# Performance work log

Hardware: AMD Instinct MI355X
Metric: run time of the kernel (lower is better)

The kernel has to match this reference:

```python
import jax, jax.numpy as jnp
import numpy as np

B, S, H = 32, 1024, 768          # batch, seq_len, bert hidden
E, W, P = 128, 8, 512            # entities/sample, span width, rel pairs/sample
NT, NR = 5, 9                    # entity types, relation types
D1, HEADS1, D2, RD = 128, 2, 64, 32
REL_IN = 2 * D2 + RD + H         # 928


def _layernorm(x, g, b):
    m = x.mean(-1, keepdims=True)
    v = x.var(-1, keepdims=True)
    return (x - m) * jax.lax.rsqrt(v + 1e-5) * g + b


def _gat_dense(x, Wm, a_src, a_dst, bias, concat):
    # Fully-connected entity graph (incl. self-loops, PyG GATConv default).
    Bn, En, _ = x.shape
    Hh, D = a_src.shape
    h = (x @ Wm).reshape(Bn, En, Hh, D)                      # [B,E,h,D]
    s = jnp.einsum('behd,hd->beh', h, a_src)                 # source score
    d = jnp.einsum('behd,hd->beh', h, a_dst)                 # target score
    # edge j->i : e_ij = leaky_relu(s_j + d_i)
    e = jax.nn.leaky_relu(d[:, :, None, :] + s[:, None, :, :], 0.2)  # [B,i,j,h]
    alpha = jax.nn.softmax(e, axis=2)
    o = jnp.einsum('bijh,bjhd->bihd', alpha, h)
    o = o.reshape(Bn, En, Hh * D) if concat else o.mean(axis=2)
    return o + bias


def setup_inputs() -> dict:
    key = jax.random.key(0)
    ks = jax.random.split(key, 20)
    f = lambda k, shape: jax.random.normal(k, shape, jnp.float32) * 0.02
    return dict(
        sequence_output=jax.random.normal(ks[0], (B, S, H), jnp.float32),
        entity_starts=jax.random.randint(ks[1], (B, E), 0, S - W),
        entity_type_ids=jax.random.randint(ks[2], (B, E), 0, NT),
        pair_idx=jax.random.randint(ks[3], (B, P, 2), 0, E),
        rel_type_ids=jax.random.randint(ks[4], (B, P), 0, NR),
        entity_type_emb=f(ks[5], (NT, H)),
        rel_type_emb=f(ks[6], (NR, RD)),
        W1=f(ks[7], (H, HEADS1 * D1)), a_src1=f(ks[8], (HEADS1, D1)),
        a_dst1=f(ks[9], (HEADS1, D1)), b1=jnp.zeros((HEADS1 * D1,), jnp.float32),
        ln1_g=jnp.ones((HEADS1 * D1,), jnp.float32), ln1_b=jnp.zeros((HEADS1 * D1,), jnp.float32),
        W2=f(ks[10], (HEADS1 * D1, D2)), a_src2=f(ks[11], (1, D2)),
        a_dst2=f(ks[12], (1, D2)), b2=jnp.zeros((D2,), jnp.float32),
        ln2_g=jnp.ones((D2,), jnp.float32), ln2_b=jnp.zeros((D2,), jnp.float32),
        Wr1=f(ks[13], (REL_IN, 256)), br1=jnp.zeros((256,), jnp.float32),
        Wr2=f(ks[14], (256, 1)), br2=jnp.zeros((1,), jnp.float32),
    )


def reference(sequence_output, entity_starts, entity_type_ids, pair_idx, rel_type_ids,
              entity_type_emb, rel_type_emb,
              W1, a_src1, a_dst1, b1, ln1_g, ln1_b,
              W2, a_src2, a_dst2, b2, ln2_g, ln2_b,
              Wr1, br1, Wr2, br2):
    bidx = jnp.arange(B)[:, None]
    # --- per-entity attention pooling over span tokens ---
    tok_idx = entity_starts[:, :, None] + jnp.arange(W)            # [B,E,W]
    toks = sequence_output[jnp.arange(B)[:, None, None], tok_idx]  # [B,E,W,H]
    mean = toks.mean(axis=2)                                       # [B,E,H]
    attn = jax.nn.softmax(jnp.einsum('bewh,beh->bew', toks, mean), axis=-1)
    pooled = jnp.einsum('bew,bewh->beh', attn, toks)
    x = pooled + entity_type_emb[entity_type_ids]                  # [B,E,H]
    # --- 2-layer GAT over fully-connected entity graph ---
    x = jax.nn.elu(_layernorm(_gat_dense(x, W1, a_src1, a_dst1, b1, True), ln1_g, ln1_b))
    x = jax.nn.elu(_layernorm(_gat_dense(x, W2, a_src2, a_dst2, b2, False), ln2_g, ln2_b))
    # --- gather-concat relation MLP scoring ---
    cls = sequence_output[:, 0, :]                                 # [B,H]
    x1 = x[bidx, pair_idx[:, :, 0]]                                # [B,P,64]
    x2 = x[bidx, pair_idx[:, :, 1]]
    rel = rel_type_emb[rel_type_ids]                               # [B,P,32]
    pv = jnp.concatenate([x1, x2, rel, jnp.broadcast_to(cls[:, None, :], (B, P, H))], axis=-1)
    scores = (jax.nn.relu(pv @ Wr1 + br1) @ Wr2 + br2)[..., 0]     # [B,P]
    return scores
```

## Files before the change

### kernel.cpp

```cpp
#include <hip/hip_runtime.h>
#include <hip/hip_bf16.h>

#define BB 32
#define SS 1024
#define HHH 768
#define EE 128
#define WW 8
#define PP 512
#define RDD 32

typedef __attribute__((ext_vector_type(8))) short bf16x8;
typedef __attribute__((ext_vector_type(8))) unsigned short us8;
typedef __attribute__((ext_vector_type(4))) unsigned short us4;
typedef __attribute__((ext_vector_type(4))) float f32x4;

__device__ __forceinline__ unsigned short f2bf(float v) {
    __hip_bfloat16 h = __float2bfloat16(v);
    return *(unsigned short*)&h;
}

__global__ __launch_bounds__(256) void pool_prep_kernel(
    const float* __restrict__ seq, const int* __restrict__ starts,
    const int* __restrict__ types, const float* __restrict__ temb,
    unsigned short* __restrict__ xout,
    const float* __restrict__ W1, unsigned short* __restrict__ Wt,
    const float* __restrict__ Wr1, unsigned short* __restrict__ Wtr,
    const float* __restrict__ W2, unsigned short* __restrict__ W2t,
    const float* __restrict__ remb, unsigned short* __restrict__ rembb,
    float* __restrict__ basep) {
    int tid = threadIdx.x;
    __shared__ float sbuf[WW * HHH];
    __shared__ float scred[WW];
    __shared__ float attn_s[WW];

    if (blockIdx.x < BB * EE) {
        int be = blockIdx.x;
        int b = be >> 7;
        int start = starts[be];
        const float4* bp4 = (const float4*)(seq + ((size_t)b * SS + start) * HHH);
        for (int idx = tid; idx < WW * (HHH / 4); idx += 256) {
            int w = idx / (HHH / 4), h4 = idx % (HHH / 4);
            float4 v = bp4[(size_t)w * (HHH / 4) + h4];
            sbuf[w * HHH + h4 * 4 + 0] = v.x; sbuf[w * HHH + h4 * 4 + 1] = v.y;
            sbuf[w * HHH + h4 * 4 + 2] = v.z; sbuf[w * HHH + h4 * 4 + 3] = v.w;
        }
        __syncthreads();

        float sc[WW];
#pragma unroll
        for (int w = 0; w < WW; w++) sc[w] = 0.f;
#pragma unroll
        for (int c = 0; c < 3; c++) {
            int h = tid + 256 * c;
            float s = 0.f;
#pragma unroll
            for (int w = 0; w < WW; w++) s += sbuf[w * HHH + h];
            float m = s * (1.0f / WW);
#pragma unroll
            for (int w = 0; w < WW; w++) sc[w] += sbuf[w * HHH + h] * m;
        }
        if (tid < WW) scred[tid] = 0.f;
        __syncthreads();
        int lane = tid & 63;
#pragma unroll
        for (int w = 0; w < WW; w++) {
            float v = sc[w];
            for (int o = 32; o > 0; o >>= 1) v += __shfl_down(v, o, 64);
            if (lane == 0) atomicAdd(&scred[w], v);
        }
        __syncthreads();
        if (tid == 0) {
            float mx = scred[0];
            for (int w = 1; w < WW; w++) mx = fmaxf(mx, scred[w]);
            float ssum = 0.f;
            float a[WW];
            for (int w = 0; w < WW; w++) { a[w] = __expf(scred[w] - mx); ssum += a[w]; }
            float inv = 1.f / ssum;
            for (int w = 0; w < WW; w++) attn_s[w] = a[w] * inv;
        }
        __syncthreads();

        int t = types[be];
        const float* emb = temb + (size_t)t * HHH;
#pragma unroll
        for (int c = 0; c < 3; c++) {
            int h = tid + 256 * c;
            float p = 0.f;
#pragma unroll
            for (int w = 0; w < WW; w++) p += attn_s[w] * sbuf[w * HHH + h];
            xout[(size_t)be * HHH + h] = f2bf(p + emb[h]);
        }
        return;
    }

    int blk = blockIdx.x - BB * EE;
    if (blk < 48) {
        int k0 = blk * 16;
        for (int i = tid; i < 16 * 256; i += 256)
            sbuf[i] = W1[(size_t)(k0 + (i >> 8)) * 256 + (i & 255)];
        __syncthreads();
        int n = tid;
        us8 v0, v1;
#pragma unroll
        for (int kk = 0; kk < 8; kk++) v0[kk] = f2bf(sbuf[kk * 256 + n]);
#pragma unroll
        for (int kk = 0; kk < 8; kk++) v1[kk] = f2bf(sbuf[(8 + kk) * 256 + n]);
        *(us8*)(Wt + (size_t)n * HHH + k0) = v0;
        *(us8*)(Wt + (size_t)n * HHH + k0 + 8) = v1;
    } else if (blk < 58) {
        int k0 = (blk - 48) * 16;
        for (int i = tid; i < 16 * 256; i += 256)
            sbuf[i] = Wr1[(size_t)(k0 + (i >> 8)) * 256 + (i & 255)];
        __syncthreads();
        int n = tid;
        us8 v0, v1;
#pragma unroll
        for (int kk = 0; kk < 8; kk++) v0[kk] = f2bf(sbuf[kk * 256 + n]);
#pragma unroll
        for (int kk = 0; kk < 8; kk++) v1[kk] = f2bf(sbuf[(8 + kk) * 256 + n]);
        *(us8*)(Wtr + (size_t)n * 160 + k0) = v0;
        *(us8*)(Wtr + (size_t)n * 160 + k0 + 8) = v1;
    } else if (blk < 74) {
        int k0 = (blk - 58) * 16;
        for (int i = tid; i < 16 * 64; i += 256)
            sbuf[(i >> 6) * 64 + (i & 63)] = W2[(size_t)(k0 + (i >> 6)) * 64 + (i & 63)];
        __syncthreads();
        if (tid < 64) {
            int n = tid;
            us8 v0, v1;
#pragma unroll
            for (int kk = 0; kk < 8; kk++) v0[kk] = f2bf(sbuf[kk * 64 + n]);
#pragma unroll
            for (int kk = 0; kk < 8; kk++) v1[kk] = f2bf(sbuf[(8 + kk) * 64 + n]);
            *(us8*)(W2t + (size_t)n * 256 + k0) = v0;
            *(us8*)(W2t + (size_t)n * 256 + k0 + 8) = v1;
        }
    } else if (blk == 74) {
        for (int i = tid; i < 9 * RDD; i += 256) rembb[i] = f2bf(remb[i]);
    } else {
        int pc = blk - 75;
        int kc = pc % 12;
        int b = pc / 12;
        int n = tid;
        if (n < 64) sbuf[4096 + n] = seq[(size_t)b * SS * HHH + kc * 64 + n];
        __syncthreads();
        float acc = 0.f;
        const float* w = Wr1 + (size_t)(160 + kc * 64) * 256 + n;
#pragma unroll 16
        for (int k = 0; k < 64; k++) acc += sbuf[4096 + k] * w[(size_t)k * 256];
        basep[((size_t)kc * 32 + b) * 256 + n] = acc;
    }
}

__global__ __launch_bounds__(256) void gemm1_mfma_kernel(
    const unsigned short* __restrict__ Xb, const unsigned short* __restrict__ Wt,
    const float* __restrict__ asrc1, const float* __restrict__ adst1,
    unsigned short* __restrict__ h1Tg,
    float* __restrict__ ps_s, float* __restrict__ ps_d) {
    const int K = HHH;
    int n0 = blockIdx.x * 64;
    int m0 = blockIdx.y * 64;
    int tid = threadIdx.x;
    int wave = tid >> 6, lane = tid & 63;
    int wm = (wave >> 1) * 32, wn = (wave & 1) * 32;

    __shared__ __align__(16) unsigned short As[64][40];
    __shared__ __align__(16) unsigned short Bs[64][40];
    __shared__ __align__(16) unsigned short T[64][72];
    __shared__ float sdred[64][2][2];

    f32x4 acc[2][2] = {};
    int ar = tid >> 2;
    int ac = (tid & 3) * 8;
    int fr = lane & 15;
    int fk = (lane >> 4) * 8;

    for (int k0 = 0; k0 < K; k0 += 32) {
        us8 av = *(const us8*)(Xb + (size_t)(m0 + ar) * K + k0 + ac);
        us8 bv = *(const us8*)(Wt + (size_t)(n0 + ar) * K + k0 + ac);
        *(us8*)(&As[ar][ac]) = av;
        *(us8*)(&Bs[ar][ac]) = bv;
        __syncthreads();

        bf16x8 a0 = *(const bf16x8*)(&As[wm + fr][fk]);
        bf16x8 a1 = *(const bf16x8*)(&As[wm + 16 + fr][fk]);
        bf16x8 b0 = *(const bf16x8*)(&Bs[wn + fr][fk]);
        bf16x8 b1 = *(const bf16x8*)(&Bs[wn + 16 + fr][fk]);

        acc[0][0] = __builtin_amdgcn_mfma_f32_16x16x32_bf16(a0, b0, acc[0][0], 0, 0, 0);
        acc[0][1] = __builtin_amdgcn_mfma_f32_16x16x32_bf16(a0, b1, acc[0][1], 0, 0, 0);
        acc[1][0] = __builtin_amdgcn_mfma_f32_16x16x32_bf16(a1, b0, acc[1][0], 0, 0, 0);
        acc[1][1] = __builtin_amdgcn_mfma_f32_16x16x32_bf16(a1, b1, acc[1][1], 0, 0, 0);
        __syncthreads();
    }

    int crow = (lane >> 4) * 4;
    int ccol = lane & 15;
    int h = n0 >> 7;
    int nb = (n0 >> 6) & 1;
    int dbase = (n0 & 127) + wn;

    float asv[2], adv[2];
#pragma unroll
    for (int ni = 0; ni < 2; ni++) {
        int d = dbase + ni * 16 + ccol;
        asv[ni] = asrc1[h * 128 + d];
        adv[ni] = adst1[h * 128 + d];
    }

#pragma unroll
    for (int mi = 0; mi < 2; mi++) {
#pragma unroll
        for (int r = 0; r < 4; r++) {
            float sp = 0.f, dp = 0.f;
#pragma unroll
            for (int ni = 0; ni < 2; ni++) {
                float v = acc[mi][ni][r];
                T[wn + ni * 16 + ccol][wm + mi * 16 + crow + r] = f2bf(v);
                sp += v * asv[ni];
                dp += v * adv[ni];
            }
            for (int msk = 1; msk < 16; msk <<= 1) {
                sp += __shfl_xor(sp, msk, 64);
                dp += __shfl_xor(dp, msk, 64);
            }
            if ((lane & 15) == 0) {
                int row = wm + mi * 16 + crow + r;
                sdred[row][wn >> 5][0] = sp;
                sdred[row][wn >> 5][1] = dp;
            }
        }
    }
    __syncthreads();

    int b = m0 >> 7;
    int j0 = m0 & 127;
    if (tid < 64) {
        float spt = sdred[tid][0][0] + sdred[tid][1][0];
        float dpt = sdred[tid][0][1] + sdred[tid][1][1];
        size_t o = (size_t)nb * 8192 + ((size_t)(m0 + tid)) * 2 + h;
        ps_s[o] = spt;
        ps_d[o] = dpt;
    }
    {
        int d_l = tid >> 2, q = tid & 3;
        us8 v0 = *(const us8*)(&T[d_l][q * 16]);
        us8 v1 = *(const us8*)(&T[d_l][q * 16 + 8]);
        size_t go = ((size_t)(b * 2 + h) * 128 + (n0 & 127) + d_l) * 128 + j0 + q * 16;
        *(us8*)(h1Tg + go) = v0;
        *(us8*)(h1Tg + go + 8) = v1;
    }
}

__global__ __launch_bounds__(256) void gat1_gemm2_kernel(
    const unsigned short* __restrict__ h1Tg,
    const float* __restrict__ ps_s, const float* __restrict__ ps_d,
    const float* __restrict__ b1, const float* __restrict__ gamma,
    const float* __restrict__ beta,
    const unsigned short* __restrict__ W2t,
    const float* __restrict__ asrc2, const float* __restrict__ adst2,
    unsigned short* __restrict__ h2Tg, float* __restrict__ s2,
    float* __restrict__ d2) {
    int b = blockIdx.x >> 2;
    int c = blockIdx.x & 3;
    int tid = threadIdx.x;
    int wave = tid >> 6, lane = tid & 63;
    int h = wave >> 1, m = wave & 1;
    int fr = lane & 15;
    int fk = (lane >> 4) * 8;

    __shared__ __align__(16) unsigned short h1T[2][128][136];
    __shared__ float ssh[2][128];
    __shared__ float dsh[2][128];
    __shared__ float lnred[32][2][2];
    __shared__ __align__(16) unsigned short g1s[32][264];
    __shared__ float sdr2[32][2][2];
    __shared__ __align__(16) unsigned short t2[64][40];

    {
        const us8* src = (const us8*)(h1Tg + (size_t)b * 32768);
#pragma unroll
        for (int it = 0; it < 16; it++) {
            int i8 = tid + it * 256;
            int row = i8 >> 4;
            int j8 = i8 & 15;
            *(us8*)(&h1T[row >> 7][row & 127][j8 * 8]) = src[i8];
        }
        int hh = tid >> 7, j = tid & 127;
        size_t o = ((size_t)b * 128 + j) * 2 + hh;
        ssh[hh][j] = ps_s[o] + ps_s[o + 8192];
        dsh[hh][j] = ps_d[o] + ps_d[o + 8192];
    }
    __syncthreads();

    bf16x8 afrag[4];
    {
        float dd = dsh[h][c * 32 + m * 16 + fr];
        float ev[4][8];
        float mx = -1e30f;
#pragma unroll
        for (int ks = 0; ks < 4; ks++)
#pragma unroll
            for (int jj = 0; jj < 8; jj++) {
                float e = dd + ssh[h][ks * 32 + fk + jj];
                e = e >= 0.f ? e : 0.2f * e;
                ev[ks][jj] = e;
                mx = fmaxf(mx, e);
            }
        mx = fmaxf(mx, __shfl_xor(mx, 16, 64));
        mx = fmaxf(mx, __shfl_xor(mx, 32, 64));
        float sm = 0.f;
#pragma unroll
        for (int ks = 0; ks < 4; ks++)
#pragma unroll
            for (int jj = 0; jj < 8; jj++) {
                float e = __expf(ev[ks][jj] - mx);
                ev[ks][jj] = e;
                sm += e;
            }
        sm += __shfl_xor(sm, 16, 64);
        sm += __shfl_xor(sm, 32, 64);
        float inv = 1.f / sm;
#pragma unroll
        for (int ks = 0; ks < 4; ks++) {
            bf16x8 a;
#pragma unroll
            for (int jj = 0; jj < 8; jj++)
                a[jj] = (short)f2bf(ev[ks][jj] * inv);
            afrag[ks] = a;
        }
    }

    f32x4 acc[8] = {};
#pragma unroll
    for (int ks = 0; ks < 4; ks++)
#pragma unroll
        for (int ni = 0; ni < 8; ni++) {
            bf16x8 bv = *(const bf16x8*)(&h1T[h][ni * 16 + fr][ks * 32 + fk]);
            acc[ni] = __builtin_amdgcn_mfma_f32_16x16x32_bf16(
                afrag[ks], bv, acc[ni], 0, 0, 0);
        }

    int crow = (lane >> 4) * 4;
    int ccol = lane & 15;
    float bv_[8], gv[8], bev[8];
#pragma unroll
    for (int ni = 0; ni < 8; ni++) {
        int d = h * 128 + ni * 16 + ccol;
        bv_[ni] = b1[d]; gv[ni] = gamma[d]; bev[ni] = beta[d];
    }
    float vv[4][8];
#pragma unroll
    for (int r = 0; r < 4; r++) {
        float s = 0.f, q = 0.f;
#pragma unroll
        for (int ni = 0; ni < 8; ni++) {
            float v = acc[ni][r] + bv_[ni];
            vv[r][ni] = v;
            s += v;
            q += v * v;
        }
        s += __shfl_xor(s, 1, 64); s += __shfl_xor(s, 2, 64);
        s += __shfl_xor(s, 4, 64); s += __shfl_xor(s, 8, 64);
        q += __shfl_xor(q, 1, 64); q += __shfl_xor(q, 2, 64);
        q += __shfl_xor(q, 4, 64); q += __shfl_xor(q, 8, 64);
        if ((lane & 15) == 0) {
            lnred[m * 16 + crow + r][h][0] = s;
            lnred[m * 16 + crow + r][h][1] = q;
        }
    }
    __syncthreads();
#pragma unroll
    for (int r = 0; r < 4; r++) {
        int row = m * 16 + crow + r;
        float s = lnred[row][0][0] + lnred[row][1][0];
        float q = lnred[row][0][1] + lnred[row][1][1];
        float mean = s * (1.f / 256.f);
        float var = q * (1.f / 256.f) - mean * mean;
        float rs = rsqrtf(var + 1e-5f);
#pragma unroll
        for (int ni = 0; ni < 8; ni++) {
            float y = (vv[r][ni] - mean) * rs * gv[ni] + bev[ni];
            y = y > 0.f ? y : (__expf(y) - 1.f);
            g1s[row][h * 128 + ni * 16 + ccol] = f2bf(y);
        }
    }
    __syncthreads();

    int m2 = wave & 1;
    int nb = wave >> 1;
    f32x4 acc2[2] = {};
#pragma unroll
    for (int kc = 0; kc < 8; kc++) {
        bf16x8 a = *(const bf16x8*)(&g1s[m2 * 16 + fr][kc * 32 + fk]);
#pragma unroll
        for (int ni = 0; ni < 2; ni++) {
            bf16x8 wv = *(const bf16x8*)(W2t + (size_t)(nb * 32 + ni * 16 + fr) * 256 +
                                         kc * 32 + fk);
            acc2[ni] = __builtin_amdgcn_mfma_f32_16x16x32_bf16(a, wv, acc2[ni], 0, 0, 0);
        }
    }
    float as2[2], ad2[2];
#pragma unroll
    for (int ni = 0; ni < 2; ni++) {
        int n = nb * 32 + ni * 16 + ccol;
        as2[ni] = asrc2[n];
        ad2[ni] = adst2[n];
    }
#pragma unroll
    for (int r = 0; r < 4; r++) {
        int rl = m2 * 16 + crow + r;
        float sp = 0.f, dp = 0.f;
#pragma unroll
        for (int ni = 0; ni < 2; ni++) {
            float v = acc2[ni][r];
            t2[nb * 32 + ni * 16 + ccol][rl] = f2bf(v);
            sp += v * as2[ni];
            dp += v * ad2[ni];
        }
        for (int msk = 1; msk < 16; msk <<= 1) {
            sp += __shfl_xor(sp, msk, 64);
            dp += __shfl_xor(dp, msk, 64);
        }
        if ((lane & 15) == 0) {
            sdr2[rl][nb][0] = sp;
            sdr2[rl][nb][1] = dp;
        }
    }
    __syncthreads();
    if (tid < 32) {
        s2[(size_t)b * 128 + c * 32 + tid] = sdr2[tid][0][0] + sdr2[tid][1][0];
        d2[(size_t)b * 128 + c * 32 + tid] = sdr2[tid][0][1] + sdr2[tid][1][1];
    }
    {
        int d = tid >> 2, q = tid & 3;
        us8 v = *(const us8*)(&t2[d][q * 8]);
        *(us8*)(h2Tg + ((size_t)b * 64 + d) * 128 + c * 32 + q * 8) = v;
    }
}

__global__ __launch_bounds__(256) void gat2_fused_kernel(
    const unsigned short* __restrict__ h2Tg, const float* __restrict__ s2,
    const float* __restrict__ d2, const float* __restrict__ b2v,
    const float* __restrict__ gamma, const float* __restrict__ beta,
    unsigned short* __restrict__ x2b) {
    int b = blockIdx.x >> 1;
    int c = blockIdx.x & 1;
    int tid = threadIdx.x;
    int wave = tid >> 6, lane = tid & 63;
    int fr = lane & 15;
    int fk = (lane >> 4) * 8;

    __shared__ __align__(16) unsigned short h2T[64][136];
    __shared__ float ssh[128];
    __shared__ float dsh[128];

    {
        const us8* src = (const us8*)(h2Tg + (size_t)b * 64 * 128);
#pragma unroll
        for (int it = 0; it < 4; it++) {
            int i8 = tid + it * 256;
            int row = i8 >> 4;
            int j8 = i8 & 15;
            *(us8*)(&h2T[row][j8 * 8]) = src[i8];
        }
        if (tid < 128) ssh[tid] = s2[(size_t)b * 128 + tid];
        else dsh[tid - 128] = d2[(size_t)b * 128 + (tid - 128)];
    }
    __syncthreads();

    bf16x8 afrag[4];
    {
        float dd = dsh[c * 64 + wave * 16 + fr];
        float ev[4][8];
        float mx = -1e30f;
#pragma unroll
        for (int ks = 0; ks < 4; ks++)
#pragma unroll
            for (int jj = 0; jj < 8; jj++) {
                float e = dd + ssh[ks * 32 + fk + jj];
                e = e >= 0.f ? e : 0.2f * e;
                ev[ks][jj] = e;
                mx = fmaxf(mx, e);
            }
        mx = fmaxf(mx, __shfl_xor(mx, 16, 64));
        mx = fmaxf(mx, __shfl_xor(mx, 32, 64));
        float sm = 0.f;
#pragma unroll
        for (int ks = 0; ks < 4; ks++)
#pragma unroll
            for (int jj = 0; jj < 8; jj++) {
                float e = __expf(ev[ks][jj] - mx);
                ev[ks][jj] = e;
                sm += e;
            }
        sm += __shfl_xor(sm, 16, 64);
        sm += __shfl_xor(sm, 32, 64);
        float inv = 1.f / sm;
#pragma unroll
        for (int ks = 0; ks < 4; ks++) {
            bf16x8 a;
#pragma unroll
            for (int jj = 0; jj < 8; jj++)
                a[jj] = (short)f2bf(ev[ks][jj] * inv);
            afrag[ks] = a;
        }
    }

    f32x4 acc[4] = {};
#pragma unroll
    for (int ks = 0; ks < 4; ks++)
#pragma unroll
        for (int ni = 0; ni < 4; ni++) {
            bf16x8 bv = *(const bf16x8*)(&h2T[ni * 16 + fr][ks * 32 + fk]);
            acc[ni] = __builtin_amdgcn_mfma_f32_16x16x32_bf16(
                afrag[ks], bv, acc[ni], 0, 0, 0);
        }

    int crow = (lane >> 4) * 4;
    int ccol = lane & 15;
    float bv_[4], gv[4], bev[4];
#pragma unroll
    for (int ni = 0; ni < 4; ni++) {
        int d = ni * 16 + ccol;
        bv_[ni] = b2v[d]; gv[ni] = gamma[d]; bev[ni] = beta[d];
    }
#pragma unroll
    for (int r = 0; r < 4; r++) {
        float v[4];
        float s = 0.f;
#pragma unroll
        for (int ni = 0; ni < 4; ni++) {
            v[ni] = acc[ni][r] + bv_[ni];
            s += v[ni];
        }
        s += __shfl_xor(s, 1, 64); s += __shfl_xor(s, 2, 64);
        s += __shfl_xor(s, 4, 64); s += __shfl_xor(s, 8, 64);
        float mean = s * (1.f / 64.f);
        float sq = 0.f;
#pragma unroll
        for (int ni = 0; ni < 4; ni++) {
            float dv = v[ni] - mean;
            sq += dv * dv;
        }
        sq += __shfl_xor(sq, 1, 64); sq += __shfl_xor(sq, 2, 64);
        sq += __shfl_xor(sq, 4, 64); sq += __shfl_xor(sq, 8, 64);
        float rs = rsqrtf(sq * (1.f / 64.f) + 1e-5f);
        int i = c * 64 + wave * 16 + crow + r;
        unsigned short* dst = x2b + (size_t)(b * 128 + i) * 64;
#pragma unroll
        for (int ni = 0; ni < 4; ni++) {
            float y = (v[ni] - mean) * rs * gv[ni] + bev[ni];
            y = y > 0.f ? y : (__expf(y) - 1.f);
            dst[ni * 16 + ccol] = f2bf(y);
        }
    }
}

__global__ __launch_bounds__(256) void score_mfma_kernel(
    const unsigned short* __restrict__ x2b, const float* __restrict__ basep,
    const float* __restrict__ br1,
    const int* __restrict__ pair_idx, const int* __restrict__ rel_ids,
    const unsigned short* __restrict__ rembb, const unsigned short* __restrict__ Wtr,
    const float* __restrict__ Wr2, const float* __restrict__ br2,
    float* __restrict__ out) {
    int blk = blockIdx.x;
    int b = blk >> 3;
    int p0 = (blk & 7) * 64;
    int tid = threadIdx.x;
    int wave = tid >> 6, lane = tid & 63;
    int wn = wave * 64;

    __shared__ __align__(16) unsigned short As[64][168];
    __shared__ __align__(16) unsigned short Bs[256][40];
    __shared__ float sred[64][4];
    __shared__ int prs[64][3];

    if (tid < 64) {
        int p = p0 + tid;
        prs[tid][0] = pair_idx[((size_t)b * PP + p) * 2 + 0];
        prs[tid][1] = pair_idx[((size_t)b * PP + p) * 2 + 1];
        prs[tid][2] = rel_ids[(size_t)b * PP + p];
    }
    __syncthreads();
    for (int it = 0; it < 10; it++) {
        int idx = tid + it * 256;
        int m = idx / 40, c = idx % 40;
        int k0 = c * 4;
        us4 v;
        if (k0 < 64)
            v = *(const us4*)(x2b + ((size_t)b * EE + prs[m][0]) * 64 + k0);
        else if (k0 < 128)
            v = *(const us4*)(x2b + ((size_t)b * EE + prs[m][1]) * 64 + (k0 - 64));
        else
            v = *(const us4*)(rembb + prs[m][2] * RDD + (k0 - 128));
        *(us4*)(&As[m][k0]) = v;
    }

    f32x4 acc[4][4] = {};
    int fr = lane & 15;
    int fk = (lane >> 4) * 8;

    for (int kc = 0; kc < 5; kc++) {
        for (int it = 0; it < 4; it++) {
            int i = tid + it * 256;
            int n = i >> 2, c = i & 3;
            *(us8*)(&Bs[n][c * 8]) =
                *(const us8*)(Wtr + (size_t)n * 160 + kc * 32 + c * 8);
        }
        __syncthreads();
        bf16x8 a[4], bv[4];
#pragma unroll
        for (int mi = 0; mi < 4; mi++)
            a[mi] = *(const bf16x8*)(&As[mi * 16 + fr][kc * 32 + fk]);
#pragma unroll
        for (int ni = 0; ni < 4; ni++)
            bv[ni] = *(const bf16x8*)(&Bs[wn + ni * 16 + fr][fk]);
#pragma unroll
        for (int mi = 0; mi < 4; mi++)
#pragma unroll
            for (int ni = 0; ni < 4; ni++)
                acc[mi][ni] = __builtin_amdgcn_mfma_f32_16x16x32_bf16(
                    a[mi], bv[ni], acc[mi][ni], 0, 0, 0);
        __syncthreads();
    }

    int crow = (lane >> 4) * 4;
    int ccol = lane & 15;
    float basev[4], w2v[4];
#pragma unroll
    for (int ni = 0; ni < 4; ni++) {
        int n = wn + ni * 16 + ccol;
        float bb = br1[n];
#pragma unroll
        for (int kc = 0; kc < 12; kc++)
            bb += basep[((size_t)kc * 32 + b) * 256 + n];
        basev[ni] = bb;
        w2v[ni] = Wr2[n];
    }
#pragma unroll
    for (int mi = 0; mi < 4; mi++) {
#pragma unroll
        for (int r = 0; r < 4; r++) {
            float p = 0.f;
#pragma unroll
            for (int ni = 0; ni < 4; ni++)
                p += fmaxf(acc[mi][ni][r] + basev[ni], 0.f) * w2v[ni];
            for (int msk = 1; msk < 16; msk <<= 1)
                p += __shfl_xor(p, msk, 64);
            if ((lane & 15) == 0)
                sred[mi * 16 + crow + r][wave] = p;
        }
    }
    __syncthreads();
    if (tid < 64) {
        float s = sred[tid][0] + sred[tid][1] + sred[tid][2] + sred[tid][3] + br2[0];
        out[(size_t)b * PP + p0 + tid] = s;
    }
}

extern "C" void kernel_launch(void* const* d_in, const int* in_sizes, int n_in,
                              void* d_out, int out_size, void* d_ws, size_t ws_size,
                              hipStream_t stream) {
    (void)in_sizes; (void)n_in; (void)out_size; (void)ws_size;
    const float* seq      = (const float*)d_in[0];
    const int*   starts   = (const int*)d_in[1];
    const int*   types    = (const int*)d_in[2];
    const int*   pair_idx = (const int*)d_in[3];
    const int*   rel_ids  = (const int*)d_in[4];
    const float* temb     = (const float*)d_in[5];
    const float* remb     = (const float*)d_in[6];
    const float* W1       = (const float*)d_in[7];
    const float* a_src1   = (const float*)d_in[8];
    const float* a_dst1   = (const float*)d_in[9];
    const float* b1       = (const float*)d_in[10];
    const float* ln1_g    = (const float*)d_in[11];
    const float* ln1_b    = (const float*)d_in[12];
    const float* W2       = (const float*)d_in[13];
    const float* a_src2   = (const float*)d_in[14];
    const float* a_dst2   = (const float*)d_in[15];
    const float* b2       = (const float*)d_in[16];
    const float* ln2_g    = (const float*)d_in[17];
    const float* ln2_b    = (const float*)d_in[18];
    const float* Wr1      = (const float*)d_in[19];
    const float* br1      = (const float*)d_in[20];
    const float* Wr2      = (const float*)d_in[21];
    const float* br2      = (const float*)d_in[22];
    float* out = (float*)d_out;

    unsigned short* xb    = (unsigned short*)d_ws;
    unsigned short* Wt    = xb + (size_t)4096 * 768;
    unsigned short* Wtr   = Wt + (size_t)256 * 768;
    unsigned short* W2t   = Wtr + (size_t)256 * 160;
    unsigned short* rembb = W2t + (size_t)64 * 256;
    unsigned short* h1Tg  = rembb + 512;
    unsigned short* h2Tg  = h1Tg + (size_t)4096 * 256;
    unsigned short* x2b   = h2Tg + (size_t)32 * 64 * 128;
    float* fbase = (float*)(x2b + (size_t)4096 * 64);
    float* ps_s  = fbase;
    float* ps_d  = ps_s + 2 * 8192;
    float* s2    = ps_d + 2 * 8192;
    float* d2    = s2 + 4096;
    float* basep = d2 + 4096;

    pool_prep_kernel<<<BB * EE + 75 + 12 * 32, 256, 0, stream>>>(
        seq, starts, types, temb, xb, W1, Wt, Wr1, Wtr, W2, W2t, remb, rembb, basep);
    gemm1_mfma_kernel<<<dim3(4, 64), 256, 0, stream>>>(xb, Wt, a_src1, a_dst1,
                                                       h1Tg, ps_s, ps_d);
    gat1_gemm2_kernel<<<BB * 4, 256, 0, stream>>>(h1Tg, ps_s, ps_d, b1, ln1_g, ln1_b,
                                                  W2t, a_src2, a_dst2, h2Tg, s2, d2);
    gat2_fused_kernel<<<BB * 2, 256, 0, stream>>>(h2Tg, s2, d2, b2, ln2_g, ln2_b, x2b);
    score_mfma_kernel<<<BB * PP / 64, 256, 0, stream>>>(x2b, basep, br1, pair_idx,
                                                        rel_ids, rembb, Wtr, Wr2,
                                                        br2, out);
}
```

Before: 228.9 us.

## Fuse four post-pooling kernels into one cooperative kernel with grid syncs

Merges the gemm1, GAT layer 1 + gemm2, GAT layer 2 and relation-scoring kernels into a single cooperative launch of 256 blocks. Each stage reuses a shared-memory union and is separated by grid-wide syncs instead of kernel boundaries. The aim is to remove the launch overhead and tail gaps of four small kernels. In exchange, the later stages must run on a fixed 256-block grid, and every grid sync carries a cost.

```diff
diff --git a/kernel.cpp b/kernel.cpp
--- a/kernel.cpp
+++ b/kernel.cpp
@@ -1,5 +1,8 @@
 #include <hip/hip_runtime.h>
 #include <hip/hip_bf16.h>
+#include <hip/hip_cooperative_groups.h>
+
+namespace cg = cooperative_groups;
 
 #define BB 32
 #define SS 1024
@@ -152,510 +155,509 @@
     }
 }
 
-__global__ __launch_bounds__(256) void gemm1_mfma_kernel(
-    const unsigned short* __restrict__ Xb, const unsigned short* __restrict__ Wt,
-    const float* __restrict__ asrc1, const float* __restrict__ adst1,
-    unsigned short* __restrict__ h1Tg,
-    float* __restrict__ ps_s, float* __restrict__ ps_d) {
-    const int K = HHH;
-    int n0 = blockIdx.x * 64;
-    int m0 = blockIdx.y * 64;
-    int tid = threadIdx.x;
-    int wave = tid >> 6, lane = tid & 63;
-    int wm = (wave >> 1) * 32, wn = (wave & 1) * 32;
-
-    __shared__ __align__(16) unsigned short As[64][40];
-    __shared__ __align__(16) unsigned short Bs[64][40];
-    __shared__ __align__(16) unsigned short T[64][72];
-    __shared__ float sdred[64][2][2];
-
-    f32x4 acc[2][2] = {};
-    int ar = tid >> 2;
-    int ac = (tid & 3) * 8;
-    int fr = lane & 15;
-    int fk = (lane >> 4) * 8;
-
-    for (int k0 = 0; k0 < K; k0 += 32) {
-        us8 av = *(const us8*)(Xb + (size_t)(m0 + ar) * K + k0 + ac);
-        us8 bv = *(const us8*)(Wt + (size_t)(n0 + ar) * K + k0 + ac);
-        *(us8*)(&As[ar][ac]) = av;
-        *(us8*)(&Bs[ar][ac]) = bv;
-        __syncthreads();
-
-        bf16x8 a0 = *(const bf16x8*)(&As[wm + fr][fk]);
-        bf16x8 a1 = *(const bf16x8*)(&As[wm + 16 + fr][fk]);
-        bf16x8 b0 = *(const bf16x8*)(&Bs[wn + fr][fk]);
-        bf16x8 b1 = *(const bf16x8*)(&Bs[wn + 16 + fr][fk]);
-
-        acc[0][0] = __builtin_amdgcn_mfma_f32_16x16x32_bf16(a0, b0, acc[0][0], 0, 0, 0);
-        acc[0][1] = __builtin_amdgcn_mfma_f32_16x16x32_bf16(a0, b1, acc[0][1], 0, 0, 0);
-        acc[1][0] = __builtin_amdgcn_mfma_f32_16x16x32_bf16(a1, b0, acc[1][0], 0, 0, 0);
-        acc[1][1] = __builtin_amdgcn_mfma_f32_16x16x32_bf16(a1, b1, acc[1][1], 0, 0, 0);
-        __syncthreads();
-    }
-
-    int crow = (lane >> 4) * 4;
-    int ccol = lane & 15;
-    int h = n0 >> 7;
-    int nb = (n0 >> 6) & 1;
-    int dbase = (n0 & 127) + wn;
-
-    float asv[2], adv[2];
-#pragma unroll
-    for (int ni = 0; ni < 2; ni++) {
-        int d = dbase + ni * 16 + ccol;
-        asv[ni] = asrc1[h * 128 + d];
-        adv[ni] = adst1[h * 128 + d];
-    }
-
-#pragma unroll
-    for (int mi = 0; mi < 2; mi++) {
-#pragma unroll
-        for (int r = 0; r < 4; r++) {
-            float sp = 0.f, dp = 0.f;
-#pragma unroll
-            for (int ni = 0; ni < 2; ni++) {
-                float v = acc[mi][ni][r];
-                T[wn + ni * 16 + ccol][wm + mi * 16 + crow + r] = f2bf(v);
-                sp += v * asv[ni];
-                dp += v * adv[ni];
-            }
-            for (int msk = 1; msk < 16; msk <<= 1) {
-                sp += __shfl_xor(sp, msk, 64);
-                dp += __shfl_xor(dp, msk, 64);
-            }
-            if ((lane & 15) == 0) {
-                int row = wm + mi * 16 + crow + r;
-                sdred[row][wn >> 5][0] = sp;
-                sdred[row][wn >> 5][1] = dp;
-            }
-        }
-    }
-    __syncthreads();
-
-    int b = m0 >> 7;
-    int j0 = m0 & 127;
-    if (tid < 64) {
-        float spt = sdred[tid][0][0] + sdred[tid][1][0];
-        float dpt = sdred[tid][0][1] + sdred[tid][1][1];
-        size_t o = (size_t)nb * 8192 + ((size_t)(m0 + tid)) * 2 + h;
-        ps_s[o] = spt;
-        ps_d[o] = dpt;
-    }
-    {
-        int d_l = tid >> 2, q = tid & 3;
-        us8 v0 = *(const us8*)(&T[d_l][q * 16]);
-        us8 v1 = *(const us8*)(&T[d_l][q * 16 + 8]);
-        size_t go = ((size_t)(b * 2 + h) * 128 + (n0 & 127) + d_l) * 128 + j0 + q * 16;
-        *(us8*)(h1Tg + go) = v0;
-        *(us8*)(h1Tg + go + 8) = v1;
-    }
-}
-
-__global__ __launch_bounds__(256) void gat1_gemm2_kernel(
-    const unsigned short* __restrict__ h1Tg,
-    const float* __restrict__ ps_s, const float* __restrict__ ps_d,
-    const float* __restrict__ b1, const float* __restrict__ gamma,
-    const float* __restrict__ beta,
-    const unsigned short* __restrict__ W2t,
-    const float* __restrict__ asrc2, const float* __restrict__ adst2,
-    unsigned short* __restrict__ h2Tg, float* __restrict__ s2,
-    float* __restrict__ d2) {
-    int b = blockIdx.x >> 2;
-    int c = blockIdx.x & 3;
-    int tid = threadIdx.x;
-    int wave = tid >> 6, lane = tid & 63;
-    int h = wave >> 1, m = wave & 1;
-    int fr = lane & 15;
-    int fk = (lane >> 4) * 8;
-
-    __shared__ __align__(16) unsigned short h1T[2][128][136];
-    __shared__ float ssh[2][128];
-    __shared__ float dsh[2][128];
-    __shared__ float lnred[32][2][2];
-    __shared__ __align__(16) unsigned short g1s[32][264];
-    __shared__ float sdr2[32][2][2];
-    __shared__ __align__(16) unsigned short t2[64][40];
-
-    {
-        const us8* src = (const us8*)(h1Tg + (size_t)b * 32768);
-#pragma unroll
-        for (int it = 0; it < 16; it++) {
-            int i8 = tid + it * 256;
-            int row = i8 >> 4;
-            int j8 = i8 & 15;
-            *(us8*)(&h1T[row >> 7][row & 127][j8 * 8]) = src[i8];
-        }
-        int hh = tid >> 7, j = tid & 127;
-        size_t o = ((size_t)b * 128 + j) * 2 + hh;
-        ssh[hh][j] = ps_s[o] + ps_s[o + 8192];
-        dsh[hh][j] = ps_d[o] + ps_d[o + 8192];
-    }
-    __syncthreads();
-
-    bf16x8 afrag[4];
-    {
-        float dd = dsh[h][c * 32 + m * 16 + fr];
-        float ev[4][8];
-        float mx = -1e30f;
-#pragma unroll
-        for (int ks = 0; ks < 4; ks++)
-#pragma unroll
-            for (int jj = 0; jj < 8; jj++) {
-                float e = dd + ssh[h][ks * 32 + fk + jj];
-                e = e >= 0.f ? e : 0.2f * e;
-                ev[ks][jj] = e;
-                mx = fmaxf(mx, e);
-            }
-        mx = fmaxf(mx, __shfl_xor(mx, 16, 64));
-        mx = fmaxf(mx, __shfl_xor(mx, 32, 64));
-        float sm = 0.f;
-#pragma unroll
-        for (int ks = 0; ks < 4; ks++)
-#pragma unroll
-            for (int jj = 0; jj < 8; jj++) {
-                float e = __expf(ev[ks][jj] - mx);
-                ev[ks][jj] = e;
-                sm += e;
-            }
-        sm += __shfl_xor(sm, 16, 64);
-        sm += __shfl_xor(sm, 32, 64);
-        float inv = 1.f / sm;
-#pragma unroll
-        for (int ks = 0; ks < 4; ks++) {
-            bf16x8 a;
-#pragma unroll
-            for (int jj = 0; jj < 8; jj++)
-                a[jj] = (short)f2bf(ev[ks][jj] * inv);
-            afrag[ks] = a;
-        }
-    }
-
-    f32x4 acc[8] = {};
-#pragma unroll
-    for (int ks = 0; ks < 4; ks++)
-#pragma unroll
-        for (int ni = 0; ni < 8; ni++) {
-            bf16x8 bv = *(const bf16x8*)(&h1T[h][ni * 16 + fr][ks * 32 + fk]);
-            acc[ni] = __builtin_amdgcn_mfma_f32_16x16x32_bf16(
-                afrag[ks], bv, acc[ni], 0, 0, 0);
-        }
-
-    int crow = (lane >> 4) * 4;
-    int ccol = lane & 15;
-    float bv_[8], gv[8], bev[8];
-#pragma unroll
-    for (int ni = 0; ni < 8; ni++) {
-        int d = h * 128 + ni * 16 + ccol;
-        bv_[ni] = b1[d]; gv[ni] = gamma[d]; bev[ni] = beta[d];
-    }
-    float vv[4][8];
-#pragma unroll
-    for (int r = 0; r < 4; r++) {
-        float s = 0.f, q = 0.f;
-#pragma unroll
-        for (int ni = 0; ni < 8; ni++) {
-            float v = acc[ni][r] + bv_[ni];
-            vv[r][ni] = v;
-            s += v;
-            q += v * v;
-        }
-        s += __shfl_xor(s, 1, 64); s += __shfl_xor(s, 2, 64);
-        s += __shfl_xor(s, 4, 64); s += __shfl_xor(s, 8, 64);
-        q += __shfl_xor(q, 1, 64); q += __shfl_xor(q, 2, 64);
-        q += __shfl_xor(q, 4, 64); q += __shfl_xor(q, 8, 64);
-        if ((lane & 15) == 0) {
-            lnred[m * 16 + crow + r][h][0] = s;
-            lnred[m * 16 + crow + r][h][1] = q;
-        }
-    }
-    __syncthreads();
-#pragma unroll
-    for (int r = 0; r < 4; r++) {
-        int row = m * 16 + crow + r;
-        float s = lnred[row][0][0] + lnred[row][1][0];
-        float q = lnred[row][0][1] + lnred[row][1][1];
-        float mean = s * (1.f / 256.f);
-        float var = q * (1.f / 256.f) - mean * mean;
-        float rs = rsqrtf(var + 1e-5f);
-#pragma unroll
-        for (int ni = 0; ni < 8; ni++) {
-            float y = (vv[r][ni] - mean) * rs * gv[ni] + bev[ni];
-            y = y > 0.f ? y : (__expf(y) - 1.f);
-            g1s[row][h * 128 + ni * 16 + ccol] = f2bf(y);
-        }
-    }
-    __syncthreads();
-
-    int m2 = wave & 1;
-    int nb = wave >> 1;
-    f32x4 acc2[2] = {};
-#pragma unroll
-    for (int kc = 0; kc < 8; kc++) {
-        bf16x8 a = *(const bf16x8*)(&g1s[m2 * 16 + fr][kc * 32 + fk]);
-#pragma unroll
-        for (int ni = 0; ni < 2; ni++) {
-            bf16x8 wv = *(const bf16x8*)(W2t + (size_t)(nb * 32 + ni * 16 + fr) * 256 +
-                                         kc * 32 + fk);
-            acc2[ni] = __builtin_amdgcn_mfma_f32_16x16x32_bf16(a, wv, acc2[ni], 0, 0, 0);
-        }
-    }
-    float as2[2], ad2[2];
-#pragma unroll
-    for (int ni = 0; ni < 2; ni++) {
-        int n = nb * 32 + ni * 16 + ccol;
-        as2[ni] = asrc2[n];
-        ad2[ni] = adst2[n];
-    }
-#pragma unroll
-    for (int r = 0; r < 4; r++) {
-        int rl = m2 * 16 + crow + r;
-        float sp = 0.f, dp = 0.f;
-#pragma unroll
-        for (int ni = 0; ni < 2; ni++) {
-            float v = acc2[ni][r];
-            t2[nb * 32 + ni * 16 + ccol][rl] = f2bf(v);
-            sp += v * as2[ni];
-            dp += v * ad2[ni];
-        }
-        for (int msk = 1; msk < 16; msk <<= 1) {
-            sp += __shfl_xor(sp, msk, 64);
-            dp += __shfl_xor(dp, msk, 64);
-        }
-        if ((lane & 15) == 0) {
-            sdr2[rl][nb][0] = sp;
-            sdr2[rl][nb][1] = dp;
-        }
-    }
-    __syncthreads();
-    if (tid < 32) {
-        s2[(size_t)b * 128 + c * 32 + tid] = sdr2[tid][0][0] + sdr2[tid][1][0];
-        d2[(size_t)b * 128 + c * 32 + tid] = sdr2[tid][0][1] + sdr2[tid][1][1];
-    }
-    {
-        int d = tid >> 2, q = tid & 3;
-        us8 v = *(const us8*)(&t2[d][q * 8]);
-        *(us8*)(h2Tg + ((size_t)b * 64 + d) * 128 + c * 32 + q * 8) = v;
-    }
-}
-
-__global__ __launch_bounds__(256) void gat2_fused_kernel(
-    const unsigned short* __restrict__ h2Tg, const float* __restrict__ s2,
-    const float* __restrict__ d2, const float* __restrict__ b2v,
-    const float* __restrict__ gamma, const float* __restrict__ beta,
-    unsigned short* __restrict__ x2b) {
-    int b = blockIdx.x >> 1;
-    int c = blockIdx.x & 1;
+struct SmP1 {
+    unsigned short As[64][40];
+    unsigned short Bs[64][40];
+    unsigned short T[64][72];
+    float sdred[64][2][2];
+};
+struct SmP2 {
+    float ssh[2][128];
+    float dsh[2][128];
+    float lnred[32][2][2];
+    unsigned short g1s[32][264];
+    float sdr2[32][2][2];
+    unsigned short t2[64][40];
+};
+struct SmP3 {
+    float ssh[128];
+    float dsh[128];
+};
+struct SmP4 {
+    unsigned short As[64][168];
+    unsigned short Bs[256][40];
+    float sred[64][4];
+    int prs[64][3];
+};
+union SmU {
+    SmP1 p1;
+    SmP2 p2;
+    SmP3 p3;
+    SmP4 p4;
+};
+
+struct FusedParams {
+    const unsigned short* Xb;
+    const unsigned short* Wt;
+    const float* asrc1;
+    const float* adst1;
+    unsigned short* h1Tg;
+    float* ps_s;
+    float* ps_d;
+    const float* b1;
+    const float* ln1g;
+    const float* ln1b;
+    const unsigned short* W2t;
+    const float* asrc2;
+    const float* adst2;
+    unsigned short* h2Tg;
+    float* s2;
+    float* d2;
+    const float* b2v;
+    const float* ln2g;
+    const float* ln2b;
+    unsigned short* x2b;
+    const float* basep;
+    const float* br1;
+    const int* pair_idx;
+    const int* rel_ids;
+    const unsigned short* rembb;
+    const unsigned short* Wtr;
+    const float* Wr2;
+    const float* br2;
+    float* out;
+};
+
+__global__ __launch_bounds__(256) void fused_mid_kernel(FusedParams p) {
+    __shared__ __align__(16) SmU sm;
+    cg::grid_group grid = cg::this_grid();
+    int bid = blockIdx.x;
     int tid = threadIdx.x;
     int wave = tid >> 6, lane = tid & 63;
     int fr = lane & 15;
     int fk = (lane >> 4) * 8;
-
-    __shared__ __align__(16) unsigned short h2T[64][136];
-    __shared__ float ssh[128];
-    __shared__ float dsh[128];
-
-    {
-        const us8* src = (const us8*)(h2Tg + (size_t)b * 64 * 128);
-#pragma unroll
-        for (int it = 0; it < 4; it++) {
-            int i8 = tid + it * 256;
-            int row = i8 >> 4;
-            int j8 = i8 & 15;
-            *(us8*)(&h2T[row][j8 * 8]) = src[i8];
-        }
-        if (tid < 128) ssh[tid] = s2[(size_t)b * 128 + tid];
-        else dsh[tid - 128] = d2[(size_t)b * 128 + (tid - 128)];
-    }
-    __syncthreads();
-
-    bf16x8 afrag[4];
-    {
-        float dd = dsh[c * 64 + wave * 16 + fr];
-        float ev[4][8];
-        float mx = -1e30f;
-#pragma unroll
-        for (int ks = 0; ks < 4; ks++)
-#pragma unroll
-            for (int jj = 0; jj < 8; jj++) {
-                float e = dd + ssh[ks * 32 + fk + jj];
-                e = e >= 0.f ? e : 0.2f * e;
-                ev[ks][jj] = e;
-                mx = fmaxf(mx, e);
-            }
-        mx = fmaxf(mx, __shfl_xor(mx, 16, 64));
-        mx = fmaxf(mx, __shfl_xor(mx, 32, 64));
-        float sm = 0.f;
-#pragma unroll
-        for (int ks = 0; ks < 4; ks++)
-#pragma unroll
-            for (int jj = 0; jj < 8; jj++) {
-                float e = __expf(ev[ks][jj] - mx);
-                ev[ks][jj] = e;
-                sm += e;
-            }
-        sm += __shfl_xor(sm, 16, 64);
-        sm += __shfl_xor(sm, 32, 64);
-        float inv = 1.f / sm;
-#pragma unroll
-        for (int ks = 0; ks < 4; ks++) {
-            bf16x8 a;
-#pragma unroll
-            for (int jj = 0; jj < 8; jj++)
-                a[jj] = (short)f2bf(ev[ks][jj] * inv);
-            afrag[ks] = a;
-        }
-    }
-
-    f32x4 acc[4] = {};
-#pragma unroll
-    for (int ks = 0; ks < 4; ks++)
-#pragma unroll
-        for (int ni = 0; ni < 4; ni++) {
-            bf16x8 bv = *(const bf16x8*)(&h2T[ni * 16 + fr][ks * 32 + fk]);
-            acc[ni] = __builtin_amdgcn_mfma_f32_16x16x32_bf16(
-                afrag[ks], bv, acc[ni], 0, 0, 0);
-        }
-
     int crow = (lane >> 4) * 4;
     int ccol = lane & 15;
-    float bv_[4], gv[4], bev[4];
-#pragma unroll
-    for (int ni = 0; ni < 4; ni++) {
-        int d = ni * 16 + ccol;
-        bv_[ni] = b2v[d]; gv[ni] = gamma[d]; bev[ni] = beta[d];
+
+    {
+        const int K = HHH;
+        int n0 = (bid & 3) * 64;
+        int m0 = (bid >> 2) * 64;
+        int wm = (wave >> 1) * 32, wn = (wave & 1) * 32;
+
+        f32x4 acc[2][2] = {};
+        int ar = tid >> 2;
+        int ac = (tid & 3) * 8;
+
+        for (int k0 = 0; k0 < K; k0 += 32) {
+            us8 av = *(const us8*)(p.Xb + (size_t)(m0 + ar) * K + k0 + ac);
+            us8 bv = *(const us8*)(p.Wt + (size_t)(n0 + ar) * K + k0 + ac);
+            *(us8*)(&sm.p1.As[ar][ac]) = av;
+            *(us8*)(&sm.p1.Bs[ar][ac]) = bv;
+            __syncthreads();
+
+            bf16x8 a0 = *(const bf16x8*)(&sm.p1.As[wm + fr][fk]);
+            bf16x8 a1 = *(const bf16x8*)(&sm.p1.As[wm + 16 + fr][fk]);
+            bf16x8 b0 = *(const bf16x8*)(&sm.p1.Bs[wn + fr][fk]);
+            bf16x8 b1 = *(const bf16x8*)(&sm.p1.Bs[wn + 16 + fr][fk]);
+
+            acc[0][0] = __builtin_amdgcn_mfma_f32_16x16x32_bf16(a0, b0, acc[0][0], 0, 0, 0);
+            acc[0][1] = __builtin_amdgcn_mfma_f32_16x16x32_bf16(a0, b1, acc[0][1], 0, 0, 0);
+            acc[1][0] = __builtin_amdgcn_mfma_f32_16x16x32_bf16(a1, b0, acc[1][0], 0, 0, 0);
+            acc[1][1] = __builtin_amdgcn_mfma_f32_16x16x32_bf16(a1, b1, acc[1][1], 0, 0, 0);
+            __syncthreads();
+        }
+
+        int h = n0 >> 7;
+        int nb = (n0 >> 6) & 1;
+        int dbase = (n0 & 127) + wn;
+
+        float asv[2], adv[2];
+#pragma unroll
+        for (int ni = 0; ni < 2; ni++) {
+            int d = dbase + ni * 16 + ccol;
+            asv[ni] = p.asrc1[h * 128 + d];
+            adv[ni] = p.adst1[h * 128 + d];
+        }
+
+#pragma unroll
+        for (int mi = 0; mi < 2; mi++) {
+#pragma unroll
+            for (int r = 0; r < 4; r++) {
+                float sp = 0.f, dp = 0.f;
+#pragma unroll
+                for (int ni = 0; ni < 2; ni++) {
+                    float v = acc[mi][ni][r];
+                    sm.p1.T[wn + ni * 16 + ccol][wm + mi * 16 + crow + r] = f2bf(v);
+                    sp += v * asv[ni];
+                    dp += v * adv[ni];
+                }
+                for (int msk = 1; msk < 16; msk <<= 1) {
+                    sp += __shfl_xor(sp, msk, 64);
+                    dp += __shfl_xor(dp, msk, 64);
+                }
+                if ((lane & 15) == 0) {
+                    int row = wm + mi * 16 + crow + r;
+                    sm.p1.sdred[row][wn >> 5][0] = sp;
+                    sm.p1.sdred[row][wn >> 5][1] = dp;
+                }
+            }
+        }
+        __syncthreads();
+
+        int b = m0 >> 7;
+        int j0 = m0 & 127;
+        if (tid < 64) {
+            float spt = sm.p1.sdred[tid][0][0] + sm.p1.sdred[tid][1][0];
+            float dpt = sm.p1.sdred[tid][0][1] + sm.p1.sdred[tid][1][1];
+            size_t o = (size_t)nb * 8192 + ((size_t)(m0 + tid)) * 2 + h;
+            p.ps_s[o] = spt;
+            p.ps_d[o] = dpt;
+        }
+        {
+            int d_l = tid >> 2, q = tid & 3;
+            us8 v0 = *(const us8*)(&sm.p1.T[d_l][q * 16]);
+            us8 v1 = *(const us8*)(&sm.p1.T[d_l][q * 16 + 8]);
+            size_t go = ((size_t)(b * 2 + h) * 128 + (n0 & 127) + d_l) * 128 + j0 + q * 16;
+            *(us8*)(p.h1Tg + go) = v0;
+            *(us8*)(p.h1Tg + go + 8) = v1;
+        }
     }
-#pragma unroll
-    for (int r = 0; r < 4; r++) {
-        float v[4];
-        float s = 0.f;
+    grid.sync();
+
+    if (bid < 128) {
+        int b = bid >> 2;
+        int c = bid & 3;
+        int h = wave >> 1, m = wave & 1;
+
+        {
+            int hh = tid >> 7, j = tid & 127;
+            size_t o = ((size_t)b * 128 + j) * 2 + hh;
+            sm.p2.ssh[hh][j] = p.ps_s[o] + p.ps_s[o + 8192];
+            sm.p2.dsh[hh][j] = p.ps_d[o] + p.ps_d[o + 8192];
+        }
+        __syncthreads();
+
+        bf16x8 afrag[4];
+        {
+            float dd = sm.p2.dsh[h][c * 32 + m * 16 + fr];
+            float ev[4][8];
+            float mx = -1e30f;
+#pragma unroll
+            for (int ks = 0; ks < 4; ks++)
+#pragma unroll
+                for (int jj = 0; jj < 8; jj++) {
+                    float e = dd + sm.p2.ssh[h][ks * 32 + fk + jj];
+                    e = e >= 0.f ? e : 0.2f * e;
+                    ev[ks][jj] = e;
+                    mx = fmaxf(mx, e);
+                }
+            mx = fmaxf(mx, __shfl_xor(mx, 16, 64));
+            mx = fmaxf(mx, __shfl_xor(mx, 32, 64));
+            float sq = 0.f;
+#pragma unroll
+            for (int ks = 0; ks < 4; ks++)
+#pragma unroll
+                for (int jj = 0; jj < 8; jj++) {
+                    float e = __expf(ev[ks][jj] - mx);
+                    ev[ks][jj] = e;
+                    sq += e;
+                }
+            sq += __shfl_xor(sq, 16, 64);
+            sq += __shfl_xor(sq, 32, 64);
+            float inv = 1.f / sq;
+#pragma unroll
+            for (int ks = 0; ks < 4; ks++) {
+                bf16x8 a;
+#pragma unroll
+                for (int jj = 0; jj < 8; jj++)
+                    a[jj] = (short)f2bf(ev[ks][jj] * inv);
+                afrag[ks] = a;
+            }
+        }
+
+        const unsigned short* hb = p.h1Tg + ((size_t)(b * 2 + h) * 128) * 128;
+        f32x4 acc[8] = {};
+#pragma unroll
+        for (int ks = 0; ks < 4; ks++)
+#pragma unroll
+            for (int ni = 0; ni < 8; ni++) {
+                bf16x8 bv = *(const bf16x8*)(hb + (size_t)(ni * 16 + fr) * 128 +
+                                             ks * 32 + fk);
+                acc[ni] = __builtin_amdgcn_mfma_f32_16x16x32_bf16(
+                    afrag[ks], bv, acc[ni], 0, 0, 0);
+            }
+
+        float bv_[8], gv[8], bev[8];
+#pragma unroll
+        for (int ni = 0; ni < 8; ni++) {
+            int d = h * 128 + ni * 16 + ccol;
+            bv_[ni] = p.b1[d]; gv[ni] = p.ln1g[d]; bev[ni] = p.ln1b[d];
+        }
+        float vv[4][8];
+#pragma unroll
+        for (int r = 0; r < 4; r++) {
+            float s = 0.f, q = 0.f;
+#pragma unroll
+            for (int ni = 0; ni < 8; ni++) {
+                float v = acc[ni][r] + bv_[ni];
+                vv[r][ni] = v;
+                s += v;
+                q += v * v;
+            }
+            s += __shfl_xor(s, 1, 64); s += __shfl_xor(s, 2, 64);
+            s += __shfl_xor(s, 4, 64); s += __shfl_xor(s, 8, 64);
+            q += __shfl_xor(q, 1, 64); q += __shfl_xor(q, 2, 64);
+            q += __shfl_xor(q, 4, 64); q += __shfl_xor(q, 8, 64);
+            if ((lane & 15) == 0) {
+                sm.p2.lnred[m * 16 + crow + r][h][0] = s;
+                sm.p2.lnred[m * 16 + crow + r][h][1] = q;
+            }
+        }
+        __syncthreads();
+#pragma unroll
+        for (int r = 0; r < 4; r++) {
+            int row = m * 16 + crow + r;
+            float s = sm.p2.lnred[row][0][0] + sm.p2.lnred[row][1][0];
+            float q = sm.p2.lnred[row][0][1] + sm.p2.lnred[row][1][1];
+            float mean = s * (1.f / 256.f);
+            float var = q * (1.f / 256.f) - mean * mean;
+            float rs = rsqrtf(var + 1e-5f);
+#pragma unroll
+            for (int ni = 0; ni < 8; ni++) {
+                float y = (vv[r][ni] - mean) * rs * gv[ni] + bev[ni];
+                y = y > 0.f ? y : (__expf(y) - 1.f);
+                sm.p2.g1s[row][h * 128 + ni * 16 + ccol] = f2bf(y);
+            }
+        }
+        __syncthreads();
+
+        int m2 = wave & 1;
+        int nb = wave >> 1;
+        f32x4 acc2[2] = {};
+#pragma unroll
+        for (int kc = 0; kc < 8; kc++) {
+            bf16x8 a = *(const bf16x8*)(&sm.p2.g1s[m2 * 16 + fr][kc * 32 + fk]);
+#pragma unroll
+            for (int ni = 0; ni < 2; ni++) {
+                bf16x8 wv = *(const bf16x8*)(p.W2t + (size_t)(nb * 32 + ni * 16 + fr) * 256 +
+                                             kc * 32 + fk);
+                acc2[ni] = __builtin_amdgcn_mfma_f32_16x16x32_bf16(a, wv, acc2[ni], 0, 0, 0);
+            }
+        }
+        float as2[2], ad2[2];
+#pragma unroll
+        for (int ni = 0; ni < 2; ni++) {
+            int n = nb * 32 + ni * 16 + ccol;
+            as2[ni] = p.asrc2[n];
+            ad2[ni] = p.adst2[n];
+        }
+#pragma unroll
+        for (int r = 0; r < 4; r++) {
+            int rl = m2 * 16 + crow + r;
+            float sp = 0.f, dp = 0.f;
+#pragma unroll
+            for (int ni = 0; ni < 2; ni++) {
+                float v = acc2[ni][r];
+                sm.p2.t2[nb * 32 + ni * 16 + ccol][rl] = f2bf(v);
+                sp += v * as2[ni];
+                dp += v * ad2[ni];
+            }
+            for (int msk = 1; msk < 16; msk <<= 1) {
+                sp += __shfl_xor(sp, msk, 64);
+                dp += __shfl_xor(dp, msk, 64);
+            }
+            if ((lane & 15) == 0) {
+                sm.p2.sdr2[rl][nb][0] = sp;
+                sm.p2.sdr2[rl][nb][1] = dp;
+            }
+        }
+        __syncthreads();
+        if (tid < 32) {
+            p.s2[(size_t)b * 128 + c * 32 + tid] =
+                sm.p2.sdr2[tid][0][0] + sm.p2.sdr2[tid][1][0];
+            p.d2[(size_t)b * 128 + c * 32 + tid] =
+                sm.p2.sdr2[tid][0][1] + sm.p2.sdr2[tid][1][1];
+        }
+        {
+            int d = tid >> 2, q = tid & 3;
+            us8 v = *(const us8*)(&sm.p2.t2[d][q * 8]);
+            *(us8*)(p.h2Tg + ((size_t)b * 64 + d) * 128 + c * 32 + q * 8) = v;
+        }
+    }
+    grid.sync();
+
+    if (bid < 64) {
+        int b = bid >> 1;
+        int c = bid & 1;
+
+        {
+            if (tid < 128) sm.p3.ssh[tid] = p.s2[(size_t)b * 128 + tid];
+            else sm.p3.dsh[tid - 128] = p.d2[(size_t)b * 128 + (tid - 128)];
+        }
+        __syncthreads();
+
+        bf16x8 afrag[4];
+        {
+            float dd = sm.p3.dsh[c * 64 + wave * 16 + fr];
+            float ev[4][8];
+            float mx = -1e30f;
+#pragma unroll
+            for (int ks = 0; ks < 4; ks++)
+#pragma unroll
+                for (int jj = 0; jj < 8; jj++) {
+                    float e = dd + sm.p3.ssh[ks * 32 + fk + jj];
+                    e = e >= 0.f ? e : 0.2f * e;
+                    ev[ks][jj] = e;
+                    mx = fmaxf(mx, e);
+                }
+            mx = fmaxf(mx, __shfl_xor(mx, 16, 64));
+            mx = fmaxf(mx, __shfl_xor(mx, 32, 64));
+            float sq = 0.f;
+#pragma unroll
+            for (int ks = 0; ks < 4; ks++)
+#pragma unroll
+                for (int jj = 0; jj < 8; jj++) {
+                    float e = __expf(ev[ks][jj] - mx);
+                    ev[ks][jj] = e;
+                    sq += e;
+                }
+            sq += __shfl_xor(sq, 16, 64);
+            sq += __shfl_xor(sq, 32, 64);
+            float inv = 1.f / sq;
+#pragma unroll
+            for (int ks = 0; ks < 4; ks++) {
+                bf16x8 a;
+#pragma unroll
+                for (int jj = 0; jj < 8; jj++)
+                    a[jj] = (short)f2bf(ev[ks][jj] * inv);
+                afrag[ks] = a;
+            }
+        }
+
+        const unsigned short* hb2 = p.h2Tg + (size_t)b * 64 * 128;
+        f32x4 acc[4] = {};
+#pragma unroll
+        for (int ks = 0; ks < 4; ks++)
+#pragma unroll
+            for (int ni = 0; ni < 4; ni++) {
+                bf16x8 bv = *(const bf16x8*)(hb2 + (size_t)(ni * 16 + fr) * 128 +
+                                             ks * 32 + fk);
+                acc[ni] = __builtin_amdgcn_mfma_f32_16x16x32_bf16(
+                    afrag[ks], bv, acc[ni], 0, 0, 0);
+            }
+
+        float bv_[4], gv[4], bev[4];
 #pragma unroll
         for (int ni = 0; ni < 4; ni++) {
-            v[ni] = acc[ni][r] + bv_[ni];
-            s += v[ni];
-        }
-        s += __shfl_xor(s, 1, 64); s += __shfl_xor(s, 2, 64);
-        s += __shfl_xor(s, 4, 64); s += __shfl_xor(s, 8, 64);
-        float mean = s * (1.f / 64.f);
-        float sq = 0.f;
+            int d = ni * 16 + ccol;
+            bv_[ni] = p.b2v[d]; gv[ni] = p.ln2g[d]; bev[ni] = p.ln2b[d];
+        }
+#pragma unroll
+        for (int r = 0; r < 4; r++) {
+            float v[4];
+            float s = 0.f;
+#pragma unroll
+            for (int ni = 0; ni < 4; ni++) {
+                v[ni] = acc[ni][r] + bv_[ni];
+                s += v[ni];
+            }
+            s += __shfl_xor(s, 1, 64); s += __shfl_xor(s, 2, 64);
+            s += __shfl_xor(s, 4, 64); s += __shfl_xor(s, 8, 64);
+            float mean = s * (1.f / 64.f);
+            float sq = 0.f;
+#pragma unroll
+            for (int ni = 0; ni < 4; ni++) {
+                float dv = v[ni] - mean;
+                sq += dv * dv;
+            }
+            sq += __shfl_xor(sq, 1, 64); sq += __shfl_xor(sq, 2, 64);
+            sq += __shfl_xor(sq, 4, 64); sq += __shfl_xor(sq, 8, 64);
+            float rs = rsqrtf(sq * (1.f / 64.f) + 1e-5f);
+            int i = c * 64 + wave * 16 + crow + r;
+            unsigned short* dst = p.x2b + (size_t)(b * 128 + i) * 64;
+#pragma unroll
+            for (int ni = 0; ni < 4; ni++) {
+                float y = (v[ni] - mean) * rs * gv[ni] + bev[ni];
+                y = y > 0.f ? y : (__expf(y) - 1.f);
+                dst[ni * 16 + ccol] = f2bf(y);
+            }
+        }
+    }
+    grid.sync();
+
+    {
+        int b = bid >> 3;
+        int p0 = (bid & 7) * 64;
+        int wn = wave * 64;
+
+        if (tid < 64) {
+            int pp = p0 + tid;
+            sm.p4.prs[tid][0] = p.pair_idx[((size_t)b * PP + pp) * 2 + 0];
+            sm.p4.prs[tid][1] = p.pair_idx[((size_t)b * PP + pp) * 2 + 1];
+            sm.p4.prs[tid][2] = p.rel_ids[(size_t)b * PP + pp];
+        }
+        __syncthreads();
+        for (int it = 0; it < 10; it++) {
+            int idx = tid + it * 256;
+            int m = idx / 40, c = idx % 40;
+            int k0 = c * 4;
+            us4 v;
+            if (k0 < 64)
+                v = *(const us4*)(p.x2b + ((size_t)b * EE + sm.p4.prs[m][0]) * 64 + k0);
+            else if (k0 < 128)
+                v = *(const us4*)(p.x2b + ((size_t)b * EE + sm.p4.prs[m][1]) * 64 + (k0 - 64));
+            else
+                v = *(const us4*)(p.rembb + sm.p4.prs[m][2] * RDD + (k0 - 128));
+            *(us4*)(&sm.p4.As[m][k0]) = v;
+        }
+
+        f32x4 acc[4][4] = {};
+        for (int kc = 0; kc < 5; kc++) {
+            for (int it = 0; it < 4; it++) {
+                int i = tid + it * 256;
+                int n = i >> 2, c = i & 3;
+                *(us8*)(&sm.p4.Bs[n][c * 8]) =
+                    *(const us8*)(p.Wtr + (size_t)n * 160 + kc * 32 + c * 8);
+            }
+            __syncthreads();
+            bf16x8 a[4], bv[4];
+#pragma unroll
+            for (int mi = 0; mi < 4; mi++)
+                a[mi] = *(const bf16x8*)(&sm.p4.As[mi * 16 + fr][kc * 32 + fk]);
+#pragma unroll
+            for (int ni = 0; ni < 4; ni++)
+                bv[ni] = *(const bf16x8*)(&sm.p4.Bs[wn + ni * 16 + fr][fk]);
+#pragma unroll
+            for (int mi = 0; mi < 4; mi++)
+#pragma unroll
+                for (int ni = 0; ni < 4; ni++)
+                    acc[mi][ni] = __builtin_amdgcn_mfma_f32_16x16x32_bf16(
+                        a[mi], bv[ni], acc[mi][ni], 0, 0, 0);
+            __syncthreads();
+        }
+
+        float basev[4], w2v[4];
 #pragma unroll
         for (int ni = 0; ni < 4; ni++) {
-            float dv = v[ni] - mean;
-            sq += dv * dv;
-        }
-        sq += __shfl_xor(sq, 1, 64); sq += __shfl_xor(sq, 2, 64);
-        sq += __shfl_xor(sq, 4, 64); sq += __shfl_xor(sq, 8, 64);
-        float rs = rsqrtf(sq * (1.f / 64.f) + 1e-5f);
-        int i = c * 64 + wave * 16 + crow + r;
-        unsigned short* dst = x2b + (size_t)(b * 128 + i) * 64;
-#pragma unroll
-        for (int ni = 0; ni < 4; ni++) {
-            float y = (v[ni] - mean) * rs * gv[ni] + bev[ni];
-            y = y > 0.f ? y : (__expf(y) - 1.f);
-            dst[ni * 16 + ccol] = f2bf(y);
-        }
-    }
-}
-
-__global__ __launch_bounds__(256) void score_mfma_kernel(
-    const unsigned short* __restrict__ x2b, const float* __restrict__ basep,
-    const float* __restrict__ br1,
-    const int* __restrict__ pair_idx, const int* __restrict__ rel_ids,
-    const unsigned short* __restrict__ rembb, const unsigned short* __restrict__ Wtr,
-    const float* __restrict__ Wr2, const float* __restrict__ br2,
-    float* __restrict__ out) {
-    int blk = blockIdx.x;
-    int b = blk >> 3;
-    int p0 = (blk & 7) * 64;
-    int tid = threadIdx.x;
-    int wave = tid >> 6, lane = tid & 63;
-    int wn = wave * 64;
-
-    __shared__ __align__(16) unsigned short As[64][168];
-    __shared__ __align__(16) unsigned short Bs[256][40];
-    __shared__ float sred[64][4];
-    __shared__ int prs[64][3];
-
-    if (tid < 64) {
-        int p = p0 + tid;
-        prs[tid][0] = pair_idx[((size_t)b * PP + p) * 2 + 0];
-        prs[tid][1] = pair_idx[((size_t)b * PP + p) * 2 + 1];
-        prs[tid][2] = rel_ids[(size_t)b * PP + p];
-    }
-    __syncthreads();
-    for (int it = 0; it < 10; it++) {
-        int idx = tid + it * 256;
-        int m = idx / 40, c = idx % 40;
-        int k0 = c * 4;
-        us4 v;
-        if (k0 < 64)
-            v = *(const us4*)(x2b + ((size_t)b * EE + prs[m][0]) * 64 + k0);
-        else if (k0 < 128)
-            v = *(const us4*)(x2b + ((size_t)b * EE + prs[m][1]) * 64 + (k0 - 64));
-        else
-            v = *(const us4*)(rembb + prs[m][2] * RDD + (k0 - 128));
-        *(us4*)(&As[m][k0]) = v;
-    }
-
-    f32x4 acc[4][4] = {};
-    int fr = lane & 15;
-    int fk = (lane >> 4) * 8;
-
-    for (int kc = 0; kc < 5; kc++) {
-        for (int it = 0; it < 4; it++) {
-            int i = tid + it * 256;
-            int n = i >> 2, c = i & 3;
-            *(us8*)(&Bs[n][c * 8]) =
-                *(const us8*)(Wtr + (size_t)n * 160 + kc * 32 + c * 8);
-        }
-        __syncthreads();
-        bf16x8 a[4], bv[4];
-#pragma unroll
-        for (int mi = 0; mi < 4; mi++)
-            a[mi] = *(const bf16x8*)(&As[mi * 16 + fr][kc * 32 + fk]);
-#pragma unroll
-        for (int ni = 0; ni < 4; ni++)
-            bv[ni] = *(const bf16x8*)(&Bs[wn + ni * 16 + fr][fk]);
-#pragma unroll
-        for (int mi = 0; mi < 4; mi++)
-#pragma unroll
-            for (int ni = 0; ni < 4; ni++)
-                acc[mi][ni] = __builtin_amdgcn_mfma_f32_16x16x32_bf16(
-                    a[mi], bv[ni], acc[mi][ni], 0, 0, 0);
-        __syncthreads();
-    }
-
-    int crow = (lane >> 4) * 4;
-    int ccol = lane & 15;
-    float basev[4], w2v[4];
-#pragma unroll
-    for (int ni = 0; ni < 4; ni++) {
-        int n = wn + ni * 16 + ccol;
-        float bb = br1[n];
-#pragma unroll
-        for (int kc = 0; kc < 12; kc++)
-            bb += basep[((size_t)kc * 32 + b) * 256 + n];
-        basev[ni] = bb;
-        w2v[ni] = Wr2[n];
-    }
-#pragma unroll
-    for (int mi = 0; mi < 4; mi++) {
-#pragma unroll
-        for (int r = 0; r < 4; r++) {
-            float p = 0.f;
-#pragma unroll
-            for (int ni = 0; ni < 4; ni++)
-                p += fmaxf(acc[mi][ni][r] + basev[ni], 0.f) * w2v[ni];
-            for (int msk = 1; msk < 16; msk <<= 1)
-                p += __shfl_xor(p, msk, 64);
-            if ((lane & 15) == 0)
-                sred[mi * 16 + crow + r][wave] = p;
-        }
-    }
-    __syncthreads();
-    if (tid < 64) {
-        float s = sred[tid][0] + sred[tid][1] + sred[tid][2] + sred[tid][3] + br2[0];
-        out[(size_t)b * PP + p0 + tid] = s;
+            int n = wn + ni * 16 + ccol;
+            float bb = p.br1[n];
+#pragma unroll
+            for (int kc = 0; kc < 12; kc++)
+                bb += p.basep[((size_t)kc * 32 + b) * 256 + n];
+            basev[ni] = bb;
+            w2v[ni] = p.Wr2[n];
+        }
+#pragma unroll
+        for (int mi = 0; mi < 4; mi++) {
+#pragma unroll
+            for (int r = 0; r < 4; r++) {
+                float pv = 0.f;
+#pragma unroll
+                for (int ni = 0; ni < 4; ni++)
+                    pv += fmaxf(acc[mi][ni][r] + basev[ni], 0.f) * w2v[ni];
+                for (int msk = 1; msk < 16; msk <<= 1)
+                    pv += __shfl_xor(pv, msk, 64);
+                if ((lane & 15) == 0)
+                    sm.p4.sred[mi * 16 + crow + r][wave] = pv;
+            }
+        }
+        __syncthreads();
+        if (tid < 64) {
+            float s = sm.p4.sred[tid][0] + sm.p4.sred[tid][1] + sm.p4.sred[tid][2] +
+                      sm.p4.sred[tid][3] + p.br2[0];
+            p.out[(size_t)b * PP + p0 + tid] = s;
+        }
     }
 }
 
@@ -704,13 +706,21 @@
     float* basep = d2 + 4096;
 
     pool_prep_kernel<<<BB * EE + 75 + 12 * 32, 256, 0, stream>>>(
-        seq, starts, types, temb, xb, W1, Wt, Wr1, Wtr, W2, W2t, remb, rembb, basep);
-    gemm1_mfma_kernel<<<dim3(4, 64), 256, 0, stream>>>(xb, Wt, a_src1, a_dst1,
-                                                       h1Tg, ps_s, ps_d);
-    gat1_gemm2_kernel<<<BB * 4, 256, 0, stream>>>(h1Tg, ps_s, ps_d, b1, ln1_g, ln1_b,
-                                                  W2t, a_src2, a_dst2, h2Tg, s2, d2);
-    gat2_fused_kernel<<<BB * 2, 256, 0, stream>>>(h2Tg, s2, d2, b2, ln2_g, ln2_b, x2b);
-    score_mfma_kernel<<<BB * PP / 64, 256, 0, stream>>>(x2b, basep, br1, pair_idx,
-                                                        rel_ids, rembb, Wtr, Wr2,
-                                                        br2, out);
+        seq, starts, types, temb, xb, W1, Wt, Wr1, Wtr, W2, W2t, remb, rembb,
+        basep);
+
+    FusedParams fp;
+    fp.Xb = xb; fp.Wt = Wt; fp.asrc1 = a_src1; fp.adst1 = a_dst1;
+    fp.h1Tg = h1Tg; fp.ps_s = ps_s; fp.ps_d = ps_d;
+    fp.b1 = b1; fp.ln1g = ln1_g; fp.ln1b = ln1_b;
+    fp.W2t = W2t; fp.asrc2 = a_src2; fp.adst2 = a_dst2;
+    fp.h2Tg = h2Tg; fp.s2 = s2; fp.d2 = d2;
+    fp.b2v = b2; fp.ln2g = ln2_g; fp.ln2b = ln2_b;
+    fp.x2b = x2b; fp.basep = basep; fp.br1 = br1;
+    fp.pair_idx = pair_idx; fp.rel_ids = rel_ids;
+    fp.rembb = rembb; fp.Wtr = Wtr; fp.Wr2 = Wr2; fp.br2 = br2;
+    fp.out = out;
+    void* kargs[] = { (void*)&fp };
+    hipLaunchCooperativeKernel((const void*)fused_mid_kernel, dim3(256), dim3(256),
+                               kargs, 0, stream);
 }
```

New measurement: 370.0 us. +61.6%, slower.
